# Performance work log

Hardware: AMD Instinct MI355X
Metric: run time of the kernel (lower is better)

## Reference

```python
import jax, jax.numpy as jnp
import numpy as np

EMBED_DIM = 1024
NUM_HEADS = 16
HEAD_DIM = EMBED_DIM // NUM_HEADS


def setup_inputs() -> dict:
    key = jax.random.key(0)
    k_x, k_wq, k_bq, k_wo, k_bo = jax.random.split(key, 5)
    B, S, E = 4, 2048, EMBED_DIM
    lim_qkv = 1.0 / np.sqrt(E)
    lim_out = 1.0 / np.sqrt(E)
    return {
        "x": jax.random.normal(k_x, (B, S, E), dtype=jnp.float32),
        # nn.Linear stores weight [out, in]; we keep [in, out] for x @ W
        "w_qkv": jax.random.uniform(k_wq, (E, 3 * E), minval=-lim_qkv, maxval=lim_qkv, dtype=jnp.float32),
        "b_qkv": jax.random.uniform(k_bq, (3 * E,), minval=-lim_qkv, maxval=lim_qkv, dtype=jnp.float32),
        "w_out": jax.random.uniform(k_wo, (E, E), minval=-lim_out, maxval=lim_out, dtype=jnp.float32),
        "b_out": jax.random.uniform(k_bo, (E,), minval=-lim_out, maxval=lim_out, dtype=jnp.float32),
    }


def reference(x, w_qkv, b_qkv, w_out, b_out):
    B, S, E = x.shape
    H, D = NUM_HEADS, HEAD_DIM
    qkv = x @ w_qkv + b_qkv                       # [B, S, 3E]
    qkv = qkv.reshape(B, S, H, 3 * D)
    q, k, v = jnp.split(qkv, 3, axis=-1)          # each [B, S, H, D]
    scale = 1.0 / np.sqrt(D).astype(np.float32)
    scores = jnp.einsum("bshd,bthd->bhst", q, k) * scale  # [B, H, S, S]
    attn = jax.nn.softmax(scores, axis=-1)
    out = jnp.einsum("bhst,bthd->bshd", attn, v)  # [B, S, H, D]
    out = out.reshape(B, S, E)
    return out @ w_out + b_out
```

## Files before the change

kernel.cpp:

```cpp
#include <hip/hip_runtime.h>
#include <hip/hip_bf16.h>


typedef short bf16x8 __attribute__((ext_vector_type(8)));
typedef unsigned short u16x8 __attribute__((ext_vector_type(8)));
typedef short s16x4 __attribute__((ext_vector_type(4)));
typedef float f32x4 __attribute__((ext_vector_type(4)));

#define QSCALE 0.18033688011112042f

__device__ inline short f2bf(float f) {
    unsigned int u = __builtin_bit_cast(unsigned int, f);
    u += 0x7fffu + ((u >> 16) & 1u);
    return (short)(u >> 16);
}

__device__ inline unsigned int pack2bf(float a, float b) {
#if __has_builtin(__builtin_amdgcn_cvt_pk_bf16_f32)
    typedef __bf16 bf2 __attribute__((ext_vector_type(2)));
    bf2 v = __builtin_amdgcn_cvt_pk_bf16_f32(a, b);
    return __builtin_bit_cast(unsigned int, v);
#else
    return (unsigned int)(unsigned short)f2bf(a) |
           ((unsigned int)(unsigned short)f2bf(b) << 16);
#endif
}

__device__ inline float fast_exp2(float x) {
#if __has_builtin(__builtin_amdgcn_exp2f)
    return __builtin_amdgcn_exp2f(x);
#else
    float r;
    asm("v_exp_f32 %0, %1" : "=v"(r) : "v"(x));
    return r;
#endif
}

__device__ inline float fast_rcp(float x) {
#if __has_builtin(__builtin_amdgcn_rcpf)
    return __builtin_amdgcn_rcpf(x);
#else
    float r;
    asm("v_rcp_f32 %0, %1" : "=v"(r) : "v"(x));
    return r;
#endif
}

__device__ inline void gload_lds16(const short* g, short* l) {
    __builtin_amdgcn_global_load_lds(
        (const __attribute__((address_space(1))) unsigned int*)g,
        (__attribute__((address_space(3))) unsigned int*)l, 16, 0, 0);
}


__global__ __launch_bounds__(256) void cvt_bf16_kernel(const float* __restrict__ in,
                                                       short* __restrict__ out) {
    int i = blockIdx.x * 256 + threadIdx.x;
    const float4 a = *(const float4*)(in + (size_t)i * 8);
    const float4 b = *(const float4*)(in + (size_t)i * 8 + 4);
    unsigned int o0 = pack2bf(a.x, a.y), o1 = pack2bf(a.z, a.w);
    unsigned int o2 = pack2bf(b.x, b.y), o3 = pack2bf(b.z, b.w);
    uint4 o = {o0, o1, o2, o3};
    *(uint4*)(out + (size_t)i * 8) = o;
}

__global__ __launch_bounds__(256) void transpose_cvt_kernel(const float* __restrict__ in,
                                                            short* __restrict__ out,
                                                            int K, int N) {
    __shared__ float tile[32][33];
    int tx = threadIdx.x & 31, ty = threadIdx.x >> 5;
    int nt = blockIdx.x * 32, kt = blockIdx.y * 32;
    for (int i = 0; i < 4; ++i)
        tile[ty + i * 8][tx] = in[(size_t)(kt + ty + i * 8) * N + nt + tx];
    __syncthreads();
    for (int i = 0; i < 4; ++i)
        out[(size_t)(nt + ty + i * 8) * K + kt + tx] = f2bf(tile[tx][ty + i * 8]);
}

__global__ __launch_bounds__(256, 2) void gemm_qkv_kernel(
        const short* __restrict__ A, const short* __restrict__ Bt,
        const float* __restrict__ bias,
        short* __restrict__ Qg, short* __restrict__ Kg, short* __restrict__ Vtg) {
    __shared__ short As[128 * 64];
    __shared__ short Bs[128 * 64];
    const int t = threadIdx.x;
    const int w = t >> 6, lane = t & 63, r = lane & 15, q4 = lane >> 4;
    const int n0 = blockIdx.x * 128, m0 = blockIdx.y * 128;
    const int wm = (w & 1) * 64, wn = (w >> 1) * 64;

    f32x4 acc[4][4];
    for (int i = 0; i < 4; ++i)
        for (int j = 0; j < 4; ++j)
            acc[i][j] = (f32x4){0.f, 0.f, 0.f, 0.f};

    for (int kk = 0; kk < 1024; kk += 64) {
        for (int ii = 0; ii < 4; ++ii) {
            const int p = t + 256 * ii;
            const int row = p >> 3;
            const int gg = (p & 7) ^ (row & 7);
            gload_lds16(A + (size_t)(m0 + row) * 1024 + kk + gg * 8, &As[p * 8]);
            gload_lds16(Bt + (size_t)(n0 + row) * 1024 + kk + gg * 8, &Bs[p * 8]);
        }
        __syncthreads();
        for (int ko = 0; ko < 2; ++ko) {
            bf16x8 af[4], bfr[4];
            for (int i = 0; i < 4; ++i) {
                const int R = wm + i * 16 + r;
                af[i] = *(const bf16x8*)(&As[R * 64 + (((ko * 4 + q4) ^ (R & 7)) * 8)]);
            }
            for (int j = 0; j < 4; ++j) {
                const int R = wn + j * 16 + r;
                bfr[j] = *(const bf16x8*)(&Bs[R * 64 + (((ko * 4 + q4) ^ (R & 7)) * 8)]);
            }
            for (int i = 0; i < 4; ++i)
                for (int j = 0; j < 4; ++j)
                    acc[i][j] = __builtin_amdgcn_mfma_f32_16x16x32_bf16(af[i], bfr[j], acc[i][j], 0, 0, 0);
        }
        __syncthreads();
    }

    for (int i = 0; i < 4; ++i) {
        for (int j = 0; j < 4; ++j) {
            const int gn = n0 + wn + j * 16 + r;
            const int h = gn / 192;
            const int rr = gn - h * 192;
            const float bv = bias[gn];
            for (int g = 0; g < 4; ++g) {
                const int gm = m0 + wm + i * 16 + q4 * 4 + g;
                const int bb = gm >> 11;
                const int s2 = gm & 2047;
                float v = acc[i][j][g] + bv;
                const size_t bh = (size_t)(bb * 16 + h);
                if (rr < 64) {
                    Qg[(bh * 2048 + s2) * 64 + rr] = f2bf(v * QSCALE);
                } else if (rr < 128) {
                    Kg[(bh * 2048 + s2) * 64 + (rr - 64)] = f2bf(v);
                } else {
                    Vtg[(bh * 64 + (rr - 128)) * 2048 + s2] = f2bf(v);
                }
            }
        }
    }
}

__global__ __launch_bounds__(256, 4) void attn_kernel(
        const short* __restrict__ Qg, const short* __restrict__ Kg,
        const short* __restrict__ Vtg, short* __restrict__ Og) {
    __shared__ short Vs[2][64 * 64];
    __shared__ short Ps[128 * 64];
    const int t = threadIdx.x;
    const int w = t >> 6, lane = t & 63, r = lane & 15, q4 = lane >> 4;
    const int blk0 = blockIdx.x;
    const int blk = ((blk0 & 7) << 7) | (blk0 >> 3);
    const int qt = blk & 15;
    const int h = (blk >> 4) & 15;
    const int b = blk >> 8;
    const size_t bh = (size_t)b * 16 + h;
    const short* Qb = Qg + bh * 2048 * 64;
    const short* Kb = Kg + bh * 2048 * 64;
    const short* Vb = Vtg + bh * 64 * 2048;

    const int r1 = t >> 3, g1 = (t & 7) ^ (r1 & 7);
    const int r2 = 32 + (t >> 3), g2 = (t & 7) ^ (r2 & 7);
    const short* vptr1 = Vb + (size_t)r1 * 2048 + g1 * 8;
    const short* vptr2 = Vb + (size_t)r2 * 2048 + g2 * 8;

    const int swz = r & 7;
    const int ga = (q4 ^ swz) * 8;
    const int gb = ((4 + q4) ^ swz) * 8;

    bf16x8 qf[2][2];
    for (int qs = 0; qs < 2; ++qs) {
        const int qrow = qt * 128 + w * 32 + qs * 16 + r;
        qf[qs][0] = *(const bf16x8*)(Qb + (size_t)qrow * 64 + q4 * 8);
        qf[qs][1] = *(const bf16x8*)(Qb + (size_t)qrow * 64 + 32 + q4 * 8);
    }

    bf16x8 onesf;
    for (int i = 0; i < 8; ++i) onesf[i] = (short)0x3F80;

    f32x4 o[2][4], ol[2];
    for (int qs = 0; qs < 2; ++qs) {
        ol[qs] = (f32x4){0.f, 0.f, 0.f, 0.f};
        for (int nt = 0; nt < 4; ++nt) o[qs][nt] = (f32x4){0.f, 0.f, 0.f, 0.f};
    }

    const int pbase0 = w * 2048;
    const int pwb = pbase0 + r * 64 + (q4 & 1) * 4;
    const int pgq = q4 >> 1;
    const int prb = pbase0 + r * 64;

    const short* kfb = Kb + (size_t)r * 64 + q4 * 8;

    gload_lds16(vptr1, &Vs[0][t * 8]);
    gload_lds16(vptr2, &Vs[0][(256 + t) * 8]);
    __syncthreads();

    int buf = 0;
    for (int kt = 0; kt < 32; ++kt) {
        const int nb = buf ^ 1;

        f32x4 st[2][4];
        __builtin_amdgcn_s_setprio(1);
        for (int c = 0; c < 4; ++c) {
            const short* kp = kfb + (size_t)(kt * 64 + c * 16) * 64;
            const bf16x8 kf0 = *(const bf16x8*)(kp);
            const bf16x8 kf1 = *(const bf16x8*)(kp + 32);
            for (int qs = 0; qs < 2; ++qs) {
                f32x4 z = (f32x4){0.f, 0.f, 0.f, 0.f};
                z = __builtin_amdgcn_mfma_f32_16x16x32_bf16(kf0, qf[qs][0], z, 0, 0, 0);
                z = __builtin_amdgcn_mfma_f32_16x16x32_bf16(kf1, qf[qs][1], z, 0, 0, 0);
                st[qs][c] = z;
            }
        }
        __builtin_amdgcn_s_setprio(0);

        if (kt + 1 < 32) {
            gload_lds16(vptr1 + (kt + 1) * 64, &Vs[nb][t * 8]);
            gload_lds16(vptr2 + (kt + 1) * 64, &Vs[nb][(256 + t) * 8]);
        }

        for (int qs = 0; qs < 2; ++qs) {
            const int pb = pwb + qs * 1024;
            for (int c = 0; c < 4; ++c) {
                const float p0 = fast_exp2(st[qs][c][0]);
                const float p1 = fast_exp2(st[qs][c][1]);
                const float p2 = fast_exp2(st[qs][c][2]);
                const float p3 = fast_exp2(st[qs][c][3]);
                uint2 pk = {pack2bf(p0, p1), pack2bf(p2, p3)};
                *(uint2*)(&Ps[pb + (((c * 2 + pgq) ^ swz) * 8)]) = pk;
            }
        }
        asm volatile("s_waitcnt lgkmcnt(0)" ::: "memory");

        const short* Vl = Vs[buf];
        __builtin_amdgcn_s_setprio(1);
        for (int ko = 0; ko < 2; ++ko) {
            const int gk = (ko == 0) ? ga : gb;
            bf16x8 pf[2];
            for (int qs = 0; qs < 2; ++qs)
                pf[qs] = *(const bf16x8*)(&Ps[prb + qs * 1024 + (((ko * 4 + q4) ^ swz) * 8)]);
            for (int qs = 0; qs < 2; ++qs)
                ol[qs] = __builtin_amdgcn_mfma_f32_16x16x32_bf16(onesf, pf[qs], ol[qs], 0, 0, 0);
            for (int nt = 0; nt < 4; ++nt) {
                const bf16x8 vf = *(const bf16x8*)(&Vl[(nt * 16 + r) * 64 + gk]);
                for (int qs = 0; qs < 2; ++qs)
                    o[qs][nt] = __builtin_amdgcn_mfma_f32_16x16x32_bf16(vf, pf[qs], o[qs][nt], 0, 0, 0);
            }
        }
        __builtin_amdgcn_s_setprio(0);

        __syncthreads();
        buf = nb;
    }

    for (int qs = 0; qs < 2; ++qs) {
        const float inv = fast_rcp(ol[qs][0]);
        const int srow = qt * 128 + w * 32 + qs * 16 + r;
        const size_t base = ((size_t)(b * 2048 + srow)) * 1024 + h * 64;
        for (int nt = 0; nt < 4; ++nt) {
            uint2 pk = {pack2bf(o[qs][nt][0] * inv, o[qs][nt][1] * inv),
                        pack2bf(o[qs][nt][2] * inv, o[qs][nt][3] * inv)};
            *(uint2*)(Og + base + nt * 16 + q4 * 4) = pk;
        }
    }
}

__global__ __launch_bounds__(256, 2) void gemm_out_kernel(
        const short* __restrict__ A, const short* __restrict__ Bt,
        const float* __restrict__ bias, float* __restrict__ out) {
    __shared__ short As[128 * 64];
    __shared__ short Bs[128 * 64];
    const int t = threadIdx.x;
    const int w = t >> 6, lane = t & 63, r = lane & 15, q4 = lane >> 4;
    const int n0 = blockIdx.x * 128, m0 = blockIdx.y * 128;
    const int wm = (w & 1) * 64, wn = (w >> 1) * 64;

    f32x4 acc[4][4];
    for (int i = 0; i < 4; ++i)
        for (int j = 0; j < 4; ++j)
            acc[i][j] = (f32x4){0.f, 0.f, 0.f, 0.f};

    for (int kk = 0; kk < 1024; kk += 64) {
        for (int ii = 0; ii < 4; ++ii) {
            const int p = t + 256 * ii;
            const int row = p >> 3;
            const int gg = (p & 7) ^ (row & 7);
            gload_lds16(A + (size_t)(m0 + row) * 1024 + kk + gg * 8, &As[p * 8]);
            gload_lds16(Bt + (size_t)(n0 + row) * 1024 + kk + gg * 8, &Bs[p * 8]);
        }
        __syncthreads();
        for (int ko = 0; ko < 2; ++ko) {
            bf16x8 af[4], bfr[4];
            for (int i = 0; i < 4; ++i) {
                const int R = wm + i * 16 + r;
                af[i] = *(const bf16x8*)(&As[R * 64 + (((ko * 4 + q4) ^ (R & 7)) * 8)]);
            }
            for (int j = 0; j < 4; ++j) {
                const int R = wn + j * 16 + r;
                bfr[j] = *(const bf16x8*)(&Bs[R * 64 + (((ko * 4 + q4) ^ (R & 7)) * 8)]);
            }
            for (int i = 0; i < 4; ++i)
                for (int j = 0; j < 4; ++j)
                    acc[i][j] = __builtin_amdgcn_mfma_f32_16x16x32_bf16(af[i], bfr[j], acc[i][j], 0, 0, 0);
        }
        __syncthreads();
    }

    for (int i = 0; i < 4; ++i) {
        for (int j = 0; j < 4; ++j) {
            const int gn = n0 + wn + j * 16 + r;
            const float bv = bias[gn];
            for (int g = 0; g < 4; ++g) {
                const int gm = m0 + wm + i * 16 + q4 * 4 + g;
                out[(size_t)gm * 1024 + gn] = acc[i][j][g] + bv;
            }
        }
    }
}


extern "C" void kernel_launch(void* const* d_in, const int* in_sizes, int n_in,
                              void* d_out, int out_size, void* d_ws, size_t ws_size,
                              hipStream_t stream) {
    const float* x     = (const float*)d_in[0];
    const float* w_qkv = (const float*)d_in[1];
    const float* b_qkv = (const float*)d_in[2];
    const float* w_out = (const float*)d_in[3];
    const float* b_out = (const float*)d_in[4];
    float* out = (float*)d_out;

    char* ws = (char*)d_ws;
    short* xb    = (short*)(ws);
    short* wqkvT = (short*)(ws + 16777216);
    short* woutT = (short*)(ws + 23068672);
    short* Qg    = (short*)(ws + 25165824);
    short* Kg    = (short*)(ws + 41943040);
    short* Vtg   = (short*)(ws + 58720256);
    short* attn  = xb;

    cvt_bf16_kernel<<<4096, 256, 0, stream>>>(x, xb);
    transpose_cvt_kernel<<<dim3(96, 32), 256, 0, stream>>>(w_qkv, wqkvT, 1024, 3072);
    transpose_cvt_kernel<<<dim3(32, 32), 256, 0, stream>>>(w_out, woutT, 1024, 1024);
    gemm_qkv_kernel<<<dim3(24, 64), 256, 0, stream>>>(xb, wqkvT, b_qkv, Qg, Kg, Vtg);
    attn_kernel<<<1024, 256, 0, stream>>>(Qg, Kg, Vtg, attn);
    gemm_out_kernel<<<dim3(8, 64), 256, 0, stream>>>(attn, woutT, b_out, out);
}
```

Baseline: 312.8 us.

## Stage K tiles through double-buffered LDS and halve P scratch buffer

Each 64-row K tile is now prefetched into a double-buffered LDS array with async global-to-LDS loads, issued together with the V prefetch at the top of each iteration. Previously every wave read K fragments directly from global memory, so each K tile was fetched four times per block. The P staging buffer is cut to one 16x64 slice per wave and reused for the two query sub-tiles in turn, which lowers LDS use and keeps four blocks per CU resident. The risks are extra LDS bank traffic and added ordering constraints from the shared P slice and the lgkmcnt waits.

```diff
diff --git a/kernel.cpp b/kernel.cpp
--- a/kernel.cpp
+++ b/kernel.cpp
@@ -146,8 +146,9 @@
 __global__ __launch_bounds__(256, 4) void attn_kernel(
         const short* __restrict__ Qg, const short* __restrict__ Kg,
         const short* __restrict__ Vtg, short* __restrict__ Og) {
+    __shared__ short Ks[2][64 * 64];
     __shared__ short Vs[2][64 * 64];
-    __shared__ short Ps[128 * 64];
+    __shared__ short Ps[4 * 16 * 64];
     const int t = threadIdx.x;
     const int w = t >> 6, lane = t & 63, r = lane & 15, q4 = lane >> 4;
     const int blk0 = blockIdx.x;
@@ -162,6 +163,8 @@
 
     const int r1 = t >> 3, g1 = (t & 7) ^ (r1 & 7);
     const int r2 = 32 + (t >> 3), g2 = (t & 7) ^ (r2 & 7);
+    const short* kptr1 = Kb + r1 * 64 + g1 * 8;
+    const short* kptr2 = Kb + r2 * 64 + g2 * 8;
     const short* vptr1 = Vb + (size_t)r1 * 2048 + g1 * 8;
     const short* vptr2 = Vb + (size_t)r2 * 2048 + g2 * 8;
 
@@ -185,13 +188,13 @@
         for (int nt = 0; nt < 4; ++nt) o[qs][nt] = (f32x4){0.f, 0.f, 0.f, 0.f};
     }
 
-    const int pbase0 = w * 2048;
+    const int pbase0 = w * 1024;
     const int pwb = pbase0 + r * 64 + (q4 & 1) * 4;
     const int pgq = q4 >> 1;
     const int prb = pbase0 + r * 64;
 
-    const short* kfb = Kb + (size_t)r * 64 + q4 * 8;
-
+    gload_lds16(kptr1, &Ks[0][t * 8]);
+    gload_lds16(kptr2, &Ks[0][(256 + t) * 8]);
     gload_lds16(vptr1, &Vs[0][t * 8]);
     gload_lds16(vptr2, &Vs[0][(256 + t) * 8]);
     __syncthreads();
@@ -200,12 +203,22 @@
     for (int kt = 0; kt < 32; ++kt) {
         const int nb = buf ^ 1;
 
+        if (kt + 1 < 32) {
+            gload_lds16(kptr1 + (kt + 1) * 4096, &Ks[nb][t * 8]);
+            gload_lds16(kptr2 + (kt + 1) * 4096, &Ks[nb][(256 + t) * 8]);
+            gload_lds16(vptr1 + (kt + 1) * 64, &Vs[nb][t * 8]);
+            gload_lds16(vptr2 + (kt + 1) * 64, &Vs[nb][(256 + t) * 8]);
+        }
+
+        const short* Kl = Ks[buf];
         f32x4 st[2][4];
         __builtin_amdgcn_s_setprio(1);
+#pragma unroll
         for (int c = 0; c < 4; ++c) {
-            const short* kp = kfb + (size_t)(kt * 64 + c * 16) * 64;
-            const bf16x8 kf0 = *(const bf16x8*)(kp);
-            const bf16x8 kf1 = *(const bf16x8*)(kp + 32);
+            const int R = (c * 16 + r) * 64;
+            const bf16x8 kf0 = *(const bf16x8*)(&Kl[R + ga]);
+            const bf16x8 kf1 = *(const bf16x8*)(&Kl[R + gb]);
+#pragma unroll
             for (int qs = 0; qs < 2; ++qs) {
                 f32x4 z = (f32x4){0.f, 0.f, 0.f, 0.f};
                 z = __builtin_amdgcn_mfma_f32_16x16x32_bf16(kf0, qf[qs][0], z, 0, 0, 0);
@@ -215,37 +228,51 @@
         }
         __builtin_amdgcn_s_setprio(0);
 
-        if (kt + 1 < 32) {
-            gload_lds16(vptr1 + (kt + 1) * 64, &Vs[nb][t * 8]);
-            gload_lds16(vptr2 + (kt + 1) * 64, &Vs[nb][(256 + t) * 8]);
-        }
-
-        for (int qs = 0; qs < 2; ++qs) {
-            const int pb = pwb + qs * 1024;
+        unsigned int pk[2][4][2];
+#pragma unroll
+        for (int qs = 0; qs < 2; ++qs)
+#pragma unroll
             for (int c = 0; c < 4; ++c) {
                 const float p0 = fast_exp2(st[qs][c][0]);
                 const float p1 = fast_exp2(st[qs][c][1]);
                 const float p2 = fast_exp2(st[qs][c][2]);
                 const float p3 = fast_exp2(st[qs][c][3]);
-                uint2 pk = {pack2bf(p0, p1), pack2bf(p2, p3)};
-                *(uint2*)(&Ps[pb + (((c * 2 + pgq) ^ swz) * 8)]) = pk;
-            }
-        }
+                pk[qs][c][0] = pack2bf(p0, p1);
+                pk[qs][c][1] = pack2bf(p2, p3);
+            }
+
+#pragma unroll
+        for (int c = 0; c < 4; ++c) {
+            uint2 u = {pk[0][c][0], pk[0][c][1]};
+            *(uint2*)(&Ps[pwb + (((c * 2 + pgq) ^ swz) * 8)]) = u;
+        }
+        bf16x8 pf0[2];
+        pf0[0] = *(const bf16x8*)(&Ps[prb + ((q4 ^ swz) * 8)]);
+        pf0[1] = *(const bf16x8*)(&Ps[prb + (((4 + q4) ^ swz) * 8)]);
+#pragma unroll
+        for (int c = 0; c < 4; ++c) {
+            uint2 u = {pk[1][c][0], pk[1][c][1]};
+            *(uint2*)(&Ps[pwb + (((c * 2 + pgq) ^ swz) * 8)]) = u;
+        }
+        bf16x8 pf1[2];
+        pf1[0] = *(const bf16x8*)(&Ps[prb + ((q4 ^ swz) * 8)]);
+        pf1[1] = *(const bf16x8*)(&Ps[prb + (((4 + q4) ^ swz) * 8)]);
         asm volatile("s_waitcnt lgkmcnt(0)" ::: "memory");
 
         const short* Vl = Vs[buf];
         __builtin_amdgcn_s_setprio(1);
+#pragma unroll
         for (int ko = 0; ko < 2; ++ko) {
             const int gk = (ko == 0) ? ga : gb;
-            bf16x8 pf[2];
-            for (int qs = 0; qs < 2; ++qs)
-                pf[qs] = *(const bf16x8*)(&Ps[prb + qs * 1024 + (((ko * 4 + q4) ^ swz) * 8)]);
-            for (int qs = 0; qs < 2; ++qs)
-                ol[qs] = __builtin_amdgcn_mfma_f32_16x16x32_bf16(onesf, pf[qs], ol[qs], 0, 0, 0);
+            const bf16x8 pfa = (ko == 0) ? pf0[0] : pf0[1];
+            const bf16x8 pfb = (ko == 0) ? pf1[0] : pf1[1];
+            ol[0] = __builtin_amdgcn_mfma_f32_16x16x32_bf16(onesf, pfa, ol[0], 0, 0, 0);
+            ol[1] = __builtin_amdgcn_mfma_f32_16x16x32_bf16(onesf, pfb, ol[1], 0, 0, 0);
+#pragma unroll
             for (int nt = 0; nt < 4; ++nt) {
                 const bf16x8 vf = *(const bf16x8*)(&Vl[(nt * 16 + r) * 64 + gk]);
-                for (int qs = 0; qs < 2; ++qs)
-                    o[qs][nt] = __builtin_amdgcn_mfma_f32_16x16x32_bf16(vf, pf[qs], o[qs][nt], 0, 0, 0);
+                o[0][nt] = __builtin_amdgcn_mfma_f32_16x16x32_bf16(vf, pfa, o[0][nt], 0, 0, 0);
+                o[1][nt] = __builtin_amdgcn_mfma_f32_16x16x32_bf16(vf, pfb, o[1][nt], 0, 0, 0);
             }
         }
         __builtin_amdgcn_s_setprio(0);
@@ -259,9 +286,9 @@
         const int srow = qt * 128 + w * 32 + qs * 16 + r;
         const size_t base = ((size_t)(b * 2048 + srow)) * 1024 + h * 64;
         for (int nt = 0; nt < 4; ++nt) {
-            uint2 pk = {pack2bf(o[qs][nt][0] * inv, o[qs][nt][1] * inv),
-                        pack2bf(o[qs][nt][2] * inv, o[qs][nt][3] * inv)};
-            *(uint2*)(Og + base + nt * 16 + q4 * 4) = pk;
+            uint2 pko = {pack2bf(o[qs][nt][0] * inv, o[qs][nt][1] * inv),
+                         pack2bf(o[qs][nt][2] * inv, o[qs][nt][3] * inv)};
+            *(uint2*)(Og + base + nt * 16 + q4 * 4) = pko;
         }
     }
 }
```

New measurement: 283.4 us. 9.4% less time.
